# Performance work log

Measured on AMD Instinct MI355X. Metric: run time of the kernel, lower is better.

## Reference

```python
import jax, jax.numpy as jnp
import numpy as np

N_NODES = 100000
N_EDGES = 1000000
IN_CH, HID_CH, N_CLS = 128, 64, 40


def setup_inputs() -> dict:
    key = jax.random.key(0)
    ks = jax.random.split(key, 8)
    x = jax.random.normal(ks[0], (N_NODES, IN_CH), dtype=jnp.float32)
    edge_index = jax.random.randint(ks[1], (2, N_EDGES), 0, N_NODES, dtype=jnp.int32)
    # Glorot-ish scaled weights (ARMAConv init_weight / root_weight, K=1 stack squeezed)
    w1_init = jax.random.normal(ks[2], (IN_CH, HID_CH), dtype=jnp.float32) / np.sqrt(IN_CH)
    w1_root = jax.random.normal(ks[3], (IN_CH, HID_CH), dtype=jnp.float32) / np.sqrt(IN_CH)
    b1 = jnp.zeros((HID_CH,), dtype=jnp.float32)
    w2_init = jax.random.normal(ks[4], (HID_CH, N_CLS), dtype=jnp.float32) / np.sqrt(HID_CH)
    w2_root = jax.random.normal(ks[5], (HID_CH, N_CLS), dtype=jnp.float32) / np.sqrt(HID_CH)
    b2 = jnp.zeros((N_CLS,), dtype=jnp.float32)
    return {"x": x, "edge_index": edge_index,
            "w1_init": w1_init, "w1_root": w1_root, "b1": b1,
            "w2_init": w2_init, "w2_root": w2_root, "b2": b2}


def _arma_layer(x, row, col, norm, w_init, w_root, bias):
    # ARMAConv, num_stacks=1, num_layers=1, shared_weights=True, eval mode (dropout=id):
    # out = relu( A_hat @ (x W_init) + x W_root + b ), mean over the single stack.
    h = x @ w_init                           # [N, F_out]
    msg = norm[:, None] * h[row]             # gather from source nodes, [E, F_out]
    agg = jax.ops.segment_sum(msg, col, num_segments=N_NODES)  # scatter-add at targets
    return jax.nn.relu(agg + x @ w_root + bias)


def reference(x, edge_index, w1_init, w1_root, b1, w2_init, w2_root, b2):
    row, col = edge_index[0], edge_index[1]
    # gcn_norm, add_self_loops=False: deg over targets, norm = d^-1/2[row] * d^-1/2[col]
    deg = jax.ops.segment_sum(jnp.ones((row.shape[0],), x.dtype), col, num_segments=N_NODES)
    dinv = jnp.where(deg > 0, jax.lax.rsqrt(jnp.maximum(deg, 1e-12)), jnp.zeros_like(deg))
    norm = dinv[row] * dinv[col]
    h = _arma_layer(x, row, col, norm, w1_init, w1_root, b1)
    h = jax.nn.relu(h)  # BiARMA relu; dropout identity in eval
    return _arma_layer(h, row, col, norm, w2_init, w2_root, b2)
```

## Files before the change

kernel.cpp:

```cpp
#include <hip/hip_runtime.h>

#define N_NODES 100000
#define N_EDGES 1000000
#define IN_CH 128
#define HID_CH 64
#define N_CLS 40

#define NBUCK 782

static inline int cdiv(int a, int b) { return (a + b - 1) / b; }

using bf16x8 = __attribute__((ext_vector_type(8))) short;
using f32x4  = __attribute__((ext_vector_type(4))) float;

__device__ __forceinline__ unsigned pack_bf2(float a, float b) {
    unsigned ua = __float_as_uint(a), ub = __float_as_uint(b);
    ua += 0x7fffu + ((ua >> 16) & 1u);
    ub += 0x7fffu + ((ub >> 16) & 1u);
    return (ua >> 16) | (ub & 0xffff0000u);
}
__device__ __forceinline__ unsigned short bf16_of(float a) {
    unsigned ua = __float_as_uint(a);
    ua += 0x7fffu + ((ua >> 16) & 1u);
    return (unsigned short)(ua >> 16);
}
__device__ __forceinline__ float bf_lo(unsigned u) { return __uint_as_float(u << 16); }
__device__ __forceinline__ float bf_hi(unsigned u) { return __uint_as_float(u & 0xffff0000u); }


__global__ __launch_bounds__(256)
void bucket_count_wconv_kernel(const int* __restrict__ cols, int* __restrict__ gcount, int E,
                               const float* __restrict__ w1i, const float* __restrict__ w1r,
                               const float* __restrict__ w2i, const float* __restrict__ w2r,
                               unsigned* __restrict__ wtgA, unsigned* __restrict__ wtgB) {
    if (blockIdx.x >= 128) {
        if (wtgA == nullptr) return;
        int id = (blockIdx.x - 128) * 256 + threadIdx.x;
        if (id < 128 * 64) {
            int c = id >> 6, kp = id & 63;
            int k = kp * 2;
            const float* W = (c < 64) ? w1i : w1r;
            int cc = (c < 64) ? c : c - 64;
            float a = W[(size_t)k * 64 + cc];
            float b = W[(size_t)(k + 1) * 64 + cc];
            wtgA[c * 64 + kp] = pack_bf2(a, b);
        } else if (id < 128 * 64 + 80 * 32) {
            int j = id - 128 * 64;
            int c = j >> 5, kp = j & 31;
            int k = kp * 2;
            const float* W = (c < 40) ? w2i : w2r;
            int cc = (c < 40) ? c : c - 40;
            float a = W[(size_t)k * 40 + cc];
            float b = W[(size_t)(k + 1) * 40 + cc];
            wtgB[c * 32 + kp] = pack_bf2(a, b);
        }
        return;
    }
    __shared__ int hist[NBUCK];
    for (int i = threadIdx.x; i < NBUCK; i += 256) hist[i] = 0;
    __syncthreads();
    int per = (E + 127) / 128;
    int s = blockIdx.x * per;
    int e = min(E, s + per);
    for (int j = s + threadIdx.x; j < e; j += 256)
        atomicAdd(&hist[cols[j] >> 7], 1);
    __syncthreads();
    for (int i = threadIdx.x; i < NBUCK; i += 256)
        if (hist[i]) atomicAdd(&gcount[i], hist[i]);
}


__global__ __launch_bounds__(1024)
void scan_bucket_kernel(const int* __restrict__ gcount, int* __restrict__ boff,
                        int* __restrict__ gcursor, int* __restrict__ offsets) {
    __shared__ int part[1024];
    int t = threadIdx.x;
    part[t] = (t < NBUCK) ? gcount[t] : 0;
    __syncthreads();
    for (int off = 1; off < 1024; off <<= 1) {
        int v = (t >= off) ? part[t - off] : 0;
        __syncthreads();
        part[t] += v;
        __syncthreads();
    }
    int excl = (t > 0) ? part[t - 1] : 0;
    if (t < NBUCK) { boff[t] = excl; gcursor[t] = excl; }
    if (t == NBUCK) { boff[NBUCK] = excl; offsets[N_NODES] = excl; }
}


__global__ __launch_bounds__(256)
void bucket_scatter_kernel(const int* __restrict__ rows, const int* __restrict__ cols,
                           int* __restrict__ gcursor, int* __restrict__ pedge, int E) {
    __shared__ int cur[NBUCK];
    for (int i = threadIdx.x; i < NBUCK; i += 256) cur[i] = 0;
    __syncthreads();
    int per = (E + gridDim.x - 1) / gridDim.x;
    int s = blockIdx.x * per;
    int e = min(E, s + per);
    for (int j = s + threadIdx.x; j < e; j += 256)
        atomicAdd(&cur[cols[j] >> 7], 1);
    __syncthreads();
    for (int i = threadIdx.x; i < NBUCK; i += 256) {
        int h = cur[i];
        cur[i] = h ? atomicAdd(&gcursor[i], h) : 0;
    }
    __syncthreads();
    for (int j = s + threadIdx.x; j < e; j += 256) {
        int c = cols[j];
        int pos = atomicAdd(&cur[c >> 7], 1);
        pedge[pos] = (rows[j] << 7) | (c & 127);
    }
}


__global__ __launch_bounds__(256)
void bucket_sort_kernel(const int* __restrict__ boff, const int* __restrict__ pedge,
                        int* __restrict__ srow, int* __restrict__ offsets,
                        float* __restrict__ dinv) {
    __shared__ int cnt[128];
    __shared__ int scn[128];
    __shared__ int cur[128];
    int b = blockIdx.x, t = threadIdx.x;
    if (t < 128) cnt[t] = 0;
    __syncthreads();
    int e0 = boff[b], e1 = boff[b + 1];
    for (int j = e0 + t; j < e1; j += 256)
        atomicAdd(&cnt[pedge[j] & 127], 1);
    __syncthreads();
    if (t < 128) scn[t] = cnt[t];
    __syncthreads();
    for (int off = 1; off < 128; off <<= 1) {
        int v = 0;
        if (t < 128 && t >= off) v = scn[t - off];
        __syncthreads();
        if (t < 128) scn[t] += v;
        __syncthreads();
    }
    if (t < 128) {
        int excl = (t > 0) ? scn[t - 1] : 0;
        cur[t] = excl;
        int node = b * 128 + t;
        if (node < N_NODES) {
            offsets[node] = e0 + excl;
            dinv[node] = cnt[t] ? rsqrtf((float)cnt[t]) : 0.f;
        }
    }
    __syncthreads();
    for (int j = e0 + t; j < e1; j += 256) {
        int p = pedge[j];
        int pos = atomicAdd(&cur[p & 127], 1);
        srow[e0 + pos] = p >> 7;
    }
}


template<int K, int C1, int C2>
__launch_bounds__(256, 6)
__global__ void gemm_fat_kernel(const float* __restrict__ X,
                                const unsigned short* __restrict__ WT,
                                const float* __restrict__ Bias,
                                const float* __restrict__ dinv,
                                unsigned short* __restrict__ Y1b,
                                float* __restrict__ Y2, int N) {
    constexpr int CT = C1 + C2;
    constexpr int NT = CT / 16;
    constexpr int KS = K / 32;
    constexpr int S16 = 72;
    constexpr int SF  = 68;
    static_assert(CT % 16 == 0 && K % 32 == 0 && C1 % 8 == 0 && C2 % 4 == 0, "shape");

    __shared__ unsigned short eb16[4 * 16 * S16];
    __shared__ float          ebf [4 * 16 * SF];

    const int tid = threadIdx.x;
    const int wave = tid >> 6;
    const int lane = tid & 63;
    const int m = lane & 15;
    const int quad = lane >> 4;
    const int r0 = blockIdx.x * 64;

    const int rowA = r0 + wave * 16 + m;
    const bool va = (rowA < N);
    const float* xr = X + (size_t)rowA * K + quad * 8;

    union AFrag { uint4 u; bf16x8 v; } af[KS];
#pragma unroll
    for (int ks = 0; ks < KS; ++ks) {
        float4 v0 = make_float4(0.f, 0.f, 0.f, 0.f);
        float4 v1 = make_float4(0.f, 0.f, 0.f, 0.f);
        if (va) {
            v0 = *reinterpret_cast<const float4*>(xr + ks * 32);
            v1 = *reinterpret_cast<const float4*>(xr + ks * 32 + 4);
        }
        af[ks].u.x = pack_bf2(v0.x, v0.y);
        af[ks].u.y = pack_bf2(v0.z, v0.w);
        af[ks].u.z = pack_bf2(v1.x, v1.y);
        af[ks].u.w = pack_bf2(v1.z, v1.w);
    }

    f32x4 acc[NT];
#pragma unroll
    for (int t = 0; t < NT; ++t) acc[t] = (f32x4){0.f, 0.f, 0.f, 0.f};
#pragma unroll
    for (int ks = 0; ks < KS; ++ks) {
#pragma unroll
        for (int t = 0; t < NT; ++t) {
            bf16x8 b = *reinterpret_cast<const bf16x8*>(&WT[(size_t)(t * 16 + m) * K + ks * 32 + quad * 8]);
            acc[t] = __builtin_amdgcn_mfma_f32_16x16x32_bf16(af[ks].v, b, acc[t], 0, 0, 0);
        }
    }

    const int rbase0 = r0 + wave * 16;
    const int rbase = rbase0 + quad * 4;
    float dv[4];
#pragma unroll
    for (int reg = 0; reg < 4; ++reg)
        dv[reg] = (rbase + reg < N) ? dinv[rbase + reg] : 0.f;

    unsigned short* e16 = &eb16[wave * 16 * S16];
    float* ef = &ebf[wave * 16 * SF];
#pragma unroll
    for (int t = 0; t < NT; ++t) {
        int c = t * 16 + m;
        if (c < C1) {
#pragma unroll
            for (int reg = 0; reg < 4; ++reg)
                e16[(quad * 4 + reg) * S16 + c] = bf16_of(acc[t][reg] * dv[reg]);
        } else {
            float b = Bias[c - C1];
#pragma unroll
            for (int reg = 0; reg < 4; ++reg)
                ef[(quad * 4 + reg) * SF + (c - C1)] = acc[t][reg] + b;
        }
    }
    __syncthreads();

    constexpr int SEG1 = C1 / 8;
    for (int it = 0; it < (16 * SEG1 + 63) / 64; ++it) {
        int task = lane + it * 64;
        if (task < 16 * SEG1) {
            int row = task / SEG1, seg = task - row * SEG1;
            int gr = rbase0 + row;
            if (gr < N) {
                uint4 v = *reinterpret_cast<const uint4*>(&eb16[(wave * 16 + row) * S16 + seg * 8]);
                *reinterpret_cast<uint4*>(&Y1b[(size_t)gr * C1 + seg * 8]) = v;
            }
        }
    }
    constexpr int SEG2 = C2 / 4;
    for (int it = 0; it < (16 * SEG2 + 63) / 64; ++it) {
        int task = lane + it * 64;
        if (task < 16 * SEG2) {
            int row = task / SEG2, seg = task - row * SEG2;
            int gr = rbase0 + row;
            if (gr < N) {
                float4 v = *reinterpret_cast<const float4*>(&ebf[(wave * 16 + row) * SF + seg * 4]);
                *reinterpret_cast<float4*>(&Y2[(size_t)gr * C2 + seg * 4]) = v;
            }
        }
    }
}


template<int K, int C1, int C2>
__launch_bounds__(256)
__global__ void gemm_mfma_fused_kernel(const float* __restrict__ X,
                                       const float* __restrict__ W1,
                                       const float* __restrict__ W2,
                                       const float* __restrict__ Bias,
                                       const float* __restrict__ dinv,
                                       unsigned short* __restrict__ Y1b,
                                       float* __restrict__ Y2, int N) {
    constexpr int CT = C1 + C2;
    constexpr int NT = CT / 16;
    constexpr int KS = K / 32;
    constexpr int KP = (K + 8) / 2;
    static_assert(CT % 16 == 0 && K % 32 == 0, "shape");
    static_assert(C1 % 4 == 0 && C2 % 4 == 0, "staging vec4");

    __shared__ unsigned xb[64 * KP];
    __shared__ unsigned wt[CT * KP];
    __shared__ float dloc[64];

    const int tid = threadIdx.x;
    const int wave = tid >> 6;
    const int lane = tid & 63;
    const int m = lane & 15;
    const int quad = lane >> 4;
    const int r0 = blockIdx.x * 64;

    if (tid < 64) {
        int gr = r0 + tid;
        dloc[tid] = (gr < N) ? dinv[gr] : 0.f;
    }

    constexpr int XIT = 64 * (K / 4);
    for (int i = tid; i < XIT; i += 256) {
        int rr = i / (K / 4);
        int k4 = i - rr * (K / 4);
        int gr = r0 + rr;
        float4 v = make_float4(0.f, 0.f, 0.f, 0.f);
        if (gr < N)
            v = *reinterpret_cast<const float4*>(&X[(size_t)gr * K + k4 * 4]);
        uint2 p;
        p.x = pack_bf2(v.x, v.y);
        p.y = pack_bf2(v.z, v.w);
        *reinterpret_cast<uint2*>(&xb[rr * KP + k4 * 2]) = p;
    }

    constexpr int WIT = (K / 2) * (CT / 4);
    for (int i = tid; i < WIT; i += 256) {
        int kp = i / (CT / 4);
        int c4 = i - kp * (CT / 4);
        int k = kp * 2;
        int c = c4 * 4;
        float4 va, vb;
        if (c < C1) {
            va = *reinterpret_cast<const float4*>(&W1[(size_t)k * C1 + c]);
            vb = *reinterpret_cast<const float4*>(&W1[(size_t)(k + 1) * C1 + c]);
        } else {
            va = *reinterpret_cast<const float4*>(&W2[(size_t)k * C2 + (c - C1)]);
            vb = *reinterpret_cast<const float4*>(&W2[(size_t)(k + 1) * C2 + (c - C1)]);
        }
        wt[(c + 0) * KP + kp] = pack_bf2(va.x, vb.x);
        wt[(c + 1) * KP + kp] = pack_bf2(va.y, vb.y);
        wt[(c + 2) * KP + kp] = pack_bf2(va.z, vb.z);
        wt[(c + 3) * KP + kp] = pack_bf2(va.w, vb.w);
    }
    __syncthreads();

    const int rowbase = wave * 16;
    f32x4 acc[NT];
#pragma unroll
    for (int t = 0; t < NT; ++t) acc[t] = (f32x4){0.f, 0.f, 0.f, 0.f};

#pragma unroll
    for (int ks = 0; ks < KS; ++ks) {
        bf16x8 a = *reinterpret_cast<const bf16x8*>(&xb[(rowbase + m) * KP + ks * 16 + quad * 4]);
#pragma unroll
        for (int t = 0; t < NT; ++t) {
            bf16x8 b = *reinterpret_cast<const bf16x8*>(&wt[(t * 16 + m) * KP + ks * 16 + quad * 4]);
            acc[t] = __builtin_amdgcn_mfma_f32_16x16x32_bf16(a, b, acc[t], 0, 0, 0);
        }
    }

#pragma unroll
    for (int t = 0; t < NT; ++t) {
        int c = t * 16 + m;
        float bias = (c >= C1) ? Bias[c - C1] : 0.f;
#pragma unroll
        for (int reg = 0; reg < 4; ++reg) {
            int rl = rowbase + quad * 4 + reg;
            int r = r0 + rl;
            if (r >= N) continue;
            float v = acc[t][reg];
            if (c < C1) {
                Y1b[(size_t)r * C1 + c] = bf16_of(v * dloc[rl]);
            } else {
                Y2[(size_t)r * C2 + (c - C1)] = v + bias;
            }
        }
    }
}


template<int C>
__launch_bounds__(256)
__global__ void pull_bf16_kernel(const int* __restrict__ offsets,
                                 const int* __restrict__ srow,
                                 const float* __restrict__ dinv,
                                 const unsigned* __restrict__ H,
                                 float* __restrict__ Y, int N) {
    constexpr int TPE = C / 4;
    constexpr int CH = C / 2;
    int gid = blockIdx.x * blockDim.x + threadIdx.x;
    int node = gid / TPE;
    int lane = gid - node * TPE;
    if (node >= N) return;

    int e0 = offsets[node];
    int e1 = offsets[node + 1];
    float dc = dinv[node];

    float4 acc = make_float4(0.f, 0.f, 0.f, 0.f);
    int j = e0;
    for (; j + 4 <= e1; j += 4) {
        int r0 = srow[j + 0];
        int r1 = srow[j + 1];
        int r2 = srow[j + 2];
        int r3 = srow[j + 3];
        uint2 u0 = *reinterpret_cast<const uint2*>(&H[(size_t)r0 * CH + lane * 2]);
        uint2 u1 = *reinterpret_cast<const uint2*>(&H[(size_t)r1 * CH + lane * 2]);
        uint2 u2 = *reinterpret_cast<const uint2*>(&H[(size_t)r2 * CH + lane * 2]);
        uint2 u3 = *reinterpret_cast<const uint2*>(&H[(size_t)r3 * CH + lane * 2]);
        acc.x += (bf_lo(u0.x) + bf_lo(u1.x)) + (bf_lo(u2.x) + bf_lo(u3.x));
        acc.y += (bf_hi(u0.x) + bf_hi(u1.x)) + (bf_hi(u2.x) + bf_hi(u3.x));
        acc.z += (bf_lo(u0.y) + bf_lo(u1.y)) + (bf_lo(u2.y) + bf_lo(u3.y));
        acc.w += (bf_hi(u0.y) + bf_hi(u1.y)) + (bf_hi(u2.y) + bf_hi(u3.y));
    }
    for (; j < e1; ++j) {
        int r = srow[j];
        uint2 u = *reinterpret_cast<const uint2*>(&H[(size_t)r * CH + lane * 2]);
        acc.x += bf_lo(u.x);
        acc.y += bf_hi(u.x);
        acc.z += bf_lo(u.y);
        acc.w += bf_hi(u.y);
    }

    float4* Y4 = reinterpret_cast<float4*>(Y);
    size_t yi = (size_t)node * TPE + lane;
    float4 y = Y4[yi];
    y.x = fmaxf(fmaf(dc, acc.x, y.x), 0.f);
    y.y = fmaxf(fmaf(dc, acc.y, y.y), 0.f);
    y.z = fmaxf(fmaf(dc, acc.z, y.z), 0.f);
    y.w = fmaxf(fmaf(dc, acc.w, y.w), 0.f);
    Y4[yi] = y;
}


extern "C" void kernel_launch(void* const* d_in, const int* in_sizes, int n_in,
                              void* d_out, int out_size, void* d_ws, size_t ws_size,
                              hipStream_t stream) {
    const float* x       = (const float*)d_in[0];
    const int*   eidx    = (const int*)d_in[1];
    const float* w1_init = (const float*)d_in[2];
    const float* w1_root = (const float*)d_in[3];
    const float* b1      = (const float*)d_in[4];
    const float* w2_init = (const float*)d_in[5];
    const float* w2_root = (const float*)d_in[6];
    const float* b2      = (const float*)d_in[7];
    float* out = (float*)d_out;

    const int* rows = eidx;
    const int* cols = eidx + N_EDGES;

    int* wsi = (int*)d_ws;
    int*      gcount  = wsi;
    int*      boff    = wsi + 784;
    int*      gcursor = wsi + 1572;
    float*    dinv    = (float*)(wsi + 2360);
    int*      offsets = wsi + 102360;
    int*      srow    = wsi + 202364;
    unsigned* h0b     = (unsigned*)(wsi + 1202364);
    int*      pedge   = wsi + 1202364;
    float*    agg1    = (float*)(wsi + 4402364);
    unsigned* h2b     = h0b;
    unsigned* wtgA    = (unsigned*)(wsi + 10802364);
    unsigned* wtgB    = wtgA + 8192;
    const size_t WS_NEEDED = 10813116ull * 4ull;

    const bool have_wt = (ws_size >= WS_NEEDED);

    hipMemsetAsync(gcount, 0, 784 * sizeof(int), stream);
    bucket_count_wconv_kernel<<<170, 256, 0, stream>>>(
        cols, gcount, N_EDGES, w1_init, w1_root, w2_init, w2_root,
        have_wt ? wtgA : nullptr, have_wt ? wtgB : nullptr);
    scan_bucket_kernel<<<1, 1024, 0, stream>>>(gcount, boff, gcursor, offsets);
    bucket_scatter_kernel<<<128, 256, 0, stream>>>(rows, cols, gcursor, pedge, N_EDGES);
    bucket_sort_kernel<<<NBUCK, 256, 0, stream>>>(boff, pedge, srow, offsets, dinv);

    const int NTILES = cdiv(N_NODES, 64);

    if (have_wt) {
        gemm_fat_kernel<IN_CH, HID_CH, HID_CH><<<NTILES, 256, 0, stream>>>(
            x, (const unsigned short*)wtgA, b1, dinv, (unsigned short*)h0b, agg1, N_NODES);
        pull_bf16_kernel<HID_CH><<<cdiv(N_NODES * (HID_CH / 4), 256), 256, 0, stream>>>(
            offsets, srow, dinv, h0b, agg1, N_NODES);

        gemm_fat_kernel<HID_CH, N_CLS, N_CLS><<<NTILES, 256, 0, stream>>>(
            agg1, (const unsigned short*)wtgB, b2, dinv, (unsigned short*)h2b, out, N_NODES);
        pull_bf16_kernel<N_CLS><<<cdiv(N_NODES * (N_CLS / 4), 256), 256, 0, stream>>>(
            offsets, srow, dinv, h2b, out, N_NODES);
    } else {
        gemm_mfma_fused_kernel<IN_CH, HID_CH, HID_CH><<<NTILES, 256, 0, stream>>>(
            x, w1_init, w1_root, b1, dinv, (unsigned short*)h0b, agg1, N_NODES);
        pull_bf16_kernel<HID_CH><<<cdiv(N_NODES * (HID_CH / 4), 256), 256, 0, stream>>>(
            offsets, srow, dinv, h0b, agg1, N_NODES);
        gemm_mfma_fused_kernel<HID_CH, N_CLS, N_CLS><<<NTILES, 256, 0, stream>>>(
            agg1, w2_init, w2_root, b2, dinv, (unsigned short*)h2b, out, N_NODES);
        pull_bf16_kernel<N_CLS><<<cdiv(N_NODES * (N_CLS / 4), 256), 256, 0, stream>>>(
            offsets, srow, dinv, h2b, out, N_NODES);
    }
}
```

Measured before the change: 263.7 us.

## Fuse layer-1 neighbor pull with layer-2 MFMA GEMM into one kernel

Adds a kernel that aggregates layer-1 messages for 16 nodes per block, applies the ReLU epilogue, packs the result to bf16 in LDS and runs the layer-2 MFMA GEMM directly. It writes the scaled bf16 messages and the root+bias output, so the separate layer-2 GEMM launch and the fp32 round trip of the hidden activations through global memory go away. A separate h2 buffer is used because h0b is still being read, and the path is only taken when the workspace is large enough, otherwise the old path runs. Risks are low occupancy and small 16-row MFMA tiles that reload the weights in every block.

Result: faster. 252.9 us (-4.1%).

```diff
diff --git a/kernel.cpp b/kernel.cpp
--- a/kernel.cpp
+++ b/kernel.cpp
@@ -263,6 +263,122 @@
 }
 
 
+__global__ __launch_bounds__(256)
+void pull_gemm_fused_kernel(const int* __restrict__ offsets,
+                            const int* __restrict__ srow,
+                            const float* __restrict__ dinv,
+                            const unsigned* __restrict__ H,
+                            const float* __restrict__ Yp,
+                            const unsigned short* __restrict__ WT2,
+                            const float* __restrict__ Bias2,
+                            unsigned short* __restrict__ H2,
+                            float* __restrict__ Outp,
+                            int N) {
+    constexpr int KP = 36;
+    __shared__ unsigned xb[16 * KP];
+    __shared__ unsigned short e16[16 * 48];
+    __shared__ float epif[16 * 44];
+
+    const int tid = threadIdx.x;
+    const int node16 = tid >> 4;
+    const int lane16 = tid & 15;
+    const int gnode = blockIdx.x * 16 + node16;
+
+    float4 h1 = make_float4(0.f, 0.f, 0.f, 0.f);
+    if (gnode < N) {
+        int e0 = offsets[gnode];
+        int e1 = offsets[gnode + 1];
+        float dc = dinv[gnode];
+        float4 acc = make_float4(0.f, 0.f, 0.f, 0.f);
+        int j = e0;
+        for (; j + 4 <= e1; j += 4) {
+            int r0 = srow[j + 0];
+            int r1 = srow[j + 1];
+            int r2 = srow[j + 2];
+            int r3 = srow[j + 3];
+            uint2 u0 = *reinterpret_cast<const uint2*>(&H[(size_t)r0 * 32 + lane16 * 2]);
+            uint2 u1 = *reinterpret_cast<const uint2*>(&H[(size_t)r1 * 32 + lane16 * 2]);
+            uint2 u2 = *reinterpret_cast<const uint2*>(&H[(size_t)r2 * 32 + lane16 * 2]);
+            uint2 u3 = *reinterpret_cast<const uint2*>(&H[(size_t)r3 * 32 + lane16 * 2]);
+            acc.x += (bf_lo(u0.x) + bf_lo(u1.x)) + (bf_lo(u2.x) + bf_lo(u3.x));
+            acc.y += (bf_hi(u0.x) + bf_hi(u1.x)) + (bf_hi(u2.x) + bf_hi(u3.x));
+            acc.z += (bf_lo(u0.y) + bf_lo(u1.y)) + (bf_lo(u2.y) + bf_lo(u3.y));
+            acc.w += (bf_hi(u0.y) + bf_hi(u1.y)) + (bf_hi(u2.y) + bf_hi(u3.y));
+        }
+        for (; j < e1; ++j) {
+            int r = srow[j];
+            uint2 u = *reinterpret_cast<const uint2*>(&H[(size_t)r * 32 + lane16 * 2]);
+            acc.x += bf_lo(u.x);
+            acc.y += bf_hi(u.x);
+            acc.z += bf_lo(u.y);
+            acc.w += bf_hi(u.y);
+        }
+        float4 y = *reinterpret_cast<const float4*>(&Yp[(size_t)gnode * 64 + lane16 * 4]);
+        h1.x = fmaxf(fmaf(dc, acc.x, y.x), 0.f);
+        h1.y = fmaxf(fmaf(dc, acc.y, y.y), 0.f);
+        h1.z = fmaxf(fmaf(dc, acc.z, y.z), 0.f);
+        h1.w = fmaxf(fmaf(dc, acc.w, y.w), 0.f);
+    }
+    xb[node16 * KP + lane16 * 2]     = pack_bf2(h1.x, h1.y);
+    xb[node16 * KP + lane16 * 2 + 1] = pack_bf2(h1.z, h1.w);
+    __syncthreads();
+
+    const int wave = tid >> 6;
+    const int lane = tid & 63;
+    const int m = lane & 15;
+    const int quad = lane >> 4;
+    const int rb = blockIdx.x * 16 + quad * 4;
+
+    float dv[4];
+#pragma unroll
+    for (int reg = 0; reg < 4; ++reg)
+        dv[reg] = (rb + reg < N) ? dinv[rb + reg] : 0.f;
+
+    bf16x8 a0 = *reinterpret_cast<const bf16x8*>(&xb[m * KP + 0 * 16 + quad * 4]);
+    bf16x8 a1 = *reinterpret_cast<const bf16x8*>(&xb[m * KP + 1 * 16 + quad * 4]);
+
+#pragma unroll
+    for (int tt = 0; tt < 2; ++tt) {
+        int t = wave + tt * 4;
+        if (t >= 5) break;
+        bf16x8 b0 = *reinterpret_cast<const bf16x8*>(&WT2[(t * 16 + m) * 64 + 0 * 32 + quad * 8]);
+        bf16x8 b1 = *reinterpret_cast<const bf16x8*>(&WT2[(t * 16 + m) * 64 + 1 * 32 + quad * 8]);
+        f32x4 acc2 = (f32x4){0.f, 0.f, 0.f, 0.f};
+        acc2 = __builtin_amdgcn_mfma_f32_16x16x32_bf16(a0, b0, acc2, 0, 0, 0);
+        acc2 = __builtin_amdgcn_mfma_f32_16x16x32_bf16(a1, b1, acc2, 0, 0, 0);
+        int c = t * 16 + m;
+        if (c < 40) {
+#pragma unroll
+            for (int reg = 0; reg < 4; ++reg)
+                e16[(quad * 4 + reg) * 48 + c] = bf16_of(acc2[reg] * dv[reg]);
+        } else {
+            float bb = Bias2[c - 40];
+#pragma unroll
+            for (int reg = 0; reg < 4; ++reg)
+                epif[(quad * 4 + reg) * 44 + (c - 40)] = acc2[reg] + bb;
+        }
+    }
+    __syncthreads();
+
+    if (tid < 80) {
+        int row = tid / 5, seg = tid - row * 5;
+        int gr = blockIdx.x * 16 + row;
+        if (gr < N) {
+            uint4 v = *reinterpret_cast<const uint4*>(&e16[row * 48 + seg * 8]);
+            *reinterpret_cast<uint4*>(&H2[(size_t)gr * 40 + seg * 8]) = v;
+        }
+    }
+    if (tid < 160) {
+        int row = tid / 10, seg = tid - row * 10;
+        int gr = blockIdx.x * 16 + row;
+        if (gr < N) {
+            float4 v = *reinterpret_cast<const float4*>(&epif[row * 44 + seg * 4]);
+            *reinterpret_cast<float4*>(&Outp[(size_t)gr * 40 + seg * 4]) = v;
+        }
+    }
+}
+
+
 template<int K, int C1, int C2>
 __launch_bounds__(256)
 __global__ void gemm_mfma_fused_kernel(const float* __restrict__ X,
@@ -448,9 +564,11 @@
     unsigned* h2b     = h0b;
     unsigned* wtgA    = (unsigned*)(wsi + 10802364);
     unsigned* wtgB    = wtgA + 8192;
-    const size_t WS_NEEDED = 10813116ull * 4ull;
-
-    const bool have_wt = (ws_size >= WS_NEEDED);
+    unsigned short* h2s = (unsigned short*)(wsi + 10813116);
+    const size_t WS_B = 10813116ull * 4ull;
+    const size_t WS_A = 12813116ull * 4ull;
+
+    const bool have_wt = (ws_size >= WS_B);
 
     hipMemsetAsync(gcount, 0, 784 * sizeof(int), stream);
     bucket_count_wconv_kernel<<<170, 256, 0, stream>>>(
@@ -462,12 +580,19 @@
 
     const int NTILES = cdiv(N_NODES, 64);
 
-    if (have_wt) {
+    if (ws_size >= WS_A) {
+        gemm_fat_kernel<IN_CH, HID_CH, HID_CH><<<NTILES, 256, 0, stream>>>(
+            x, (const unsigned short*)wtgA, b1, dinv, (unsigned short*)h0b, agg1, N_NODES);
+        pull_gemm_fused_kernel<<<cdiv(N_NODES, 16), 256, 0, stream>>>(
+            offsets, srow, dinv, h0b, agg1, (const unsigned short*)wtgB, b2,
+            h2s, out, N_NODES);
+        pull_bf16_kernel<N_CLS><<<cdiv(N_NODES * (N_CLS / 4), 256), 256, 0, stream>>>(
+            offsets, srow, dinv, (const unsigned*)h2s, out, N_NODES);
+    } else if (have_wt) {
         gemm_fat_kernel<IN_CH, HID_CH, HID_CH><<<NTILES, 256, 0, stream>>>(
             x, (const unsigned short*)wtgA, b1, dinv, (unsigned short*)h0b, agg1, N_NODES);
         pull_bf16_kernel<HID_CH><<<cdiv(N_NODES * (HID_CH / 4), 256), 256, 0, stream>>>(
             offsets, srow, dinv, h0b, agg1, N_NODES);
-
         gemm_fat_kernel<HID_CH, N_CLS, N_CLS><<<NTILES, 256, 0, stream>>>(
             agg1, (const unsigned short*)wtgB, b2, dinv, (unsigned short*)h2b, out, N_NODES);
         pull_bf16_kernel<N_CLS><<<cdiv(N_NODES * (N_CLS / 4), 256), 256, 0, stream>>>(
```
